# Performance work log

Hardware: AMD Instinct MI355X
Metric: run time of the kernel (lower is better)

Reference implementation:

```python
import jax, jax.numpy as jnp
import numpy as np

H, W = 6144, 6144
KH, KW = 3, 3


def setup_inputs() -> dict:
    key = jax.random.key(0)
    k1, k2, k3 = jax.random.split(key, 3)
    x = jax.random.normal(k1, (H, W), dtype=jnp.float32)
    kernel = jax.random.normal(k2, (KH, KW), dtype=jnp.float32)
    bias = jax.random.normal(k3, (1,), dtype=jnp.float32)
    return {"x": x, "kernel": kernel, "bias": bias}


def reference(x, kernel, bias):
    # Valid 2D cross-correlation (no kernel flip), identical math to the
    # per-pixel double loop: out[i,j] = sum(x[i:i+h, j:j+w] * kernel) + bias.
    lhs = x[None, None, :, :]            # [N=1, C=1, H, W]
    rhs = kernel[None, None, :, :]       # [O=1, I=1, h, w]
    out = jax.lax.conv_general_dilated(
        lhs, rhs,
        window_strides=(1, 1),
        padding="VALID",
        dimension_numbers=("NCHW", "OIHW", "NCHW"),
    )[0, 0]                              # [H-h+1, W-w+1]
    return out + bias[0]
```

## Files before the change

kernel.cpp:

```cpp
#include <hip/hip_runtime.h>


#define W_IN  6144
#define H_IN  6144
#define OW    6142
#define OH    6142
#define ROWS  4
#define NCOLT 1536

typedef float f32x2 __attribute__((ext_vector_type(2)));
typedef float f32x4 __attribute__((ext_vector_type(4)));

template <bool INTERIOR>
__device__ __forceinline__ void corr_body(const float* __restrict__ x,
                                          float* __restrict__ out,
                                          int c0, int r0,
                                          float k00, float k01, float k02,
                                          float k10, float k11, float k12,
                                          float k20, float k21, float k22,
                                          float bv)
{
    if (c0 + 4 <= OW) {
        float v[6][6];
#pragma unroll
        for (int r = 0; r < 6; ++r) {
            const int rr = r0 + r;
            if (INTERIOR || rr < H_IN) {
                const float* p = x + rr * W_IN + c0;
                const f32x4 a = *reinterpret_cast<const f32x4*>(p);
                const f32x2 c = *reinterpret_cast<const f32x2*>(p + 4);
                v[r][0] = a.x; v[r][1] = a.y; v[r][2] = a.z; v[r][3] = a.w;
                v[r][4] = c.x; v[r][5] = c.y;
            } else {
                v[r][0] = v[r][1] = v[r][2] = v[r][3] = v[r][4] = v[r][5] = 0.f;
            }
        }
#pragma unroll
        for (int m = 0; m < ROWS; ++m) {
            const int rr = r0 + m;
            if (INTERIOR || rr < OH) {
                float acc[4];
#pragma unroll
                for (int j = 0; j < 4; ++j) {
                    acc[j] = bv
                        + v[m + 0][j] * k00 + v[m + 0][j + 1] * k01 + v[m + 0][j + 2] * k02
                        + v[m + 1][j] * k10 + v[m + 1][j + 1] * k11 + v[m + 1][j + 2] * k12
                        + v[m + 2][j] * k20 + v[m + 2][j + 1] * k21 + v[m + 2][j + 2] * k22;
                }
                float* po = out + rr * OW + c0;
                f32x2 s0; s0.x = acc[0]; s0.y = acc[1];
                f32x2 s1; s1.x = acc[2]; s1.y = acc[3];
                __builtin_nontemporal_store(s0, reinterpret_cast<f32x2*>(po));
                __builtin_nontemporal_store(s1, reinterpret_cast<f32x2*>(po + 2));
            }
        }
    } else {
        float v[6][4];
#pragma unroll
        for (int r = 0; r < 6; ++r) {
            const int rr = r0 + r;
            if (INTERIOR || rr < H_IN) {
                const f32x4 a = *reinterpret_cast<const f32x4*>(x + rr * W_IN + c0);
                v[r][0] = a.x; v[r][1] = a.y; v[r][2] = a.z; v[r][3] = a.w;
            } else {
                v[r][0] = v[r][1] = v[r][2] = v[r][3] = 0.f;
            }
        }
#pragma unroll
        for (int m = 0; m < ROWS; ++m) {
            const int rr = r0 + m;
            if (INTERIOR || rr < OH) {
                float a0 = bv
                    + v[m + 0][0] * k00 + v[m + 0][1] * k01 + v[m + 0][2] * k02
                    + v[m + 1][0] * k10 + v[m + 1][1] * k11 + v[m + 1][2] * k12
                    + v[m + 2][0] * k20 + v[m + 2][1] * k21 + v[m + 2][2] * k22;
                float a1 = bv
                    + v[m + 0][1] * k00 + v[m + 0][2] * k01 + v[m + 0][3] * k02
                    + v[m + 1][1] * k10 + v[m + 1][2] * k11 + v[m + 1][3] * k12
                    + v[m + 2][1] * k20 + v[m + 2][2] * k21 + v[m + 2][3] * k22;
                f32x2 s0; s0.x = a0; s0.y = a1;
                __builtin_nontemporal_store(s0, reinterpret_cast<f32x2*>(out + rr * OW + c0));
            }
        }
    }
}

__global__ __launch_bounds__(256, 4)
void corr2d_kernel(const float* __restrict__ x,
                   const float* __restrict__ kk,
                   const float* __restrict__ bias,
                   float* __restrict__ out) {
    const int t  = blockIdx.x * 256 + threadIdx.x;
    const int c0 = t << 2;
    const int r0 = blockIdx.y * ROWS;

    const float k00 = kk[0], k01 = kk[1], k02 = kk[2];
    const float k10 = kk[3], k11 = kk[4], k12 = kk[5];
    const float k20 = kk[6], k21 = kk[7], k22 = kk[8];
    const float bv = bias[0];

    if (r0 + ROWS + 1 < H_IN) {
        corr_body<true>(x, out, c0, r0, k00, k01, k02, k10, k11, k12, k20, k21, k22, bv);
    } else {
        corr_body<false>(x, out, c0, r0, k00, k01, k02, k10, k11, k12, k20, k21, k22, bv);
    }
}

extern "C" void kernel_launch(void* const* d_in, const int* in_sizes, int n_in,
                              void* d_out, int out_size, void* d_ws, size_t ws_size,
                              hipStream_t stream) {
    const float* x    = (const float*)d_in[0];
    const float* k    = (const float*)d_in[1];
    const float* bias = (const float*)d_in[2];
    float* out        = (float*)d_out;

    dim3 block(256, 1, 1);
    dim3 grid(NCOLT / 256, (OH + ROWS - 1) / ROWS, 1);
    corr2d_kernel<<<grid, block, 0, stream>>>(x, k, bias, out);
}
```

Baseline: 60.55 us.

## Double rows per thread and remap workgroups per XCD for locality

Each thread now computes 8 output rows instead of 4, which cuts the halo re-read overhead from 6/4 to 10/8 input rows per output row. The grid is flattened to 1D and workgroup IDs are remapped so that consecutive workgroups dispatched to the same XCD cover adjacent row tiles, improving L2 sharing of halo rows. The occupancy hint in launch_bounds is dropped. Register use rises because each thread holds 10x6 input values.

```diff
diff --git a/kernel.cpp b/kernel.cpp
--- a/kernel.cpp
+++ b/kernel.cpp
@@ -5,14 +5,17 @@
 #define H_IN  6144
 #define OW    6142
 #define OH    6142
-#define ROWS  4
-#define NCOLT 1536
+#define ROWS  8
+#define GRID_X 6
+#define GRID_Y 768
+#define NWG   (GRID_X * GRID_Y)
+#define WG_PER_XCD (NWG / 8)
 
 typedef float f32x2 __attribute__((ext_vector_type(2)));
 typedef float f32x4 __attribute__((ext_vector_type(4)));
 
 template <bool INTERIOR>
-__device__ __forceinline__ void corr_body(const float* __restrict__ x,
+__device__ __forceinline__ void body_main(const float* __restrict__ x,
                                           float* __restrict__ out,
                                           int c0, int r0,
                                           float k00, float k01, float k02,
@@ -20,89 +23,110 @@
                                           float k20, float k21, float k22,
                                           float bv)
 {
-    if (c0 + 4 <= OW) {
-        float v[6][6];
+    float v[ROWS + 2][6];
 #pragma unroll
-        for (int r = 0; r < 6; ++r) {
-            const int rr = r0 + r;
-            if (INTERIOR || rr < H_IN) {
-                const float* p = x + rr * W_IN + c0;
-                const f32x4 a = *reinterpret_cast<const f32x4*>(p);
-                const f32x2 c = *reinterpret_cast<const f32x2*>(p + 4);
-                v[r][0] = a.x; v[r][1] = a.y; v[r][2] = a.z; v[r][3] = a.w;
-                v[r][4] = c.x; v[r][5] = c.y;
-            } else {
-                v[r][0] = v[r][1] = v[r][2] = v[r][3] = v[r][4] = v[r][5] = 0.f;
+    for (int r = 0; r < ROWS + 2; ++r) {
+        const int rr = r0 + r;
+        if (INTERIOR || rr < H_IN) {
+            const float* p = x + rr * W_IN + c0;
+            const f32x4 a = *reinterpret_cast<const f32x4*>(p);
+            const f32x2 c = *reinterpret_cast<const f32x2*>(p + 4);
+            v[r][0] = a.x; v[r][1] = a.y; v[r][2] = a.z; v[r][3] = a.w;
+            v[r][4] = c.x; v[r][5] = c.y;
+        } else {
+#pragma unroll
+            for (int j = 0; j < 6; ++j) v[r][j] = 0.f;
+        }
+    }
+
+#pragma unroll
+    for (int m = 0; m < ROWS; ++m) {
+        const int rr = r0 + m;
+        if (INTERIOR || rr < OH) {
+            float acc[4];
+#pragma unroll
+            for (int j = 0; j < 4; ++j) {
+                acc[j] = bv
+                    + v[m + 0][j] * k00 + v[m + 0][j + 1] * k01 + v[m + 0][j + 2] * k02
+                    + v[m + 1][j] * k10 + v[m + 1][j + 1] * k11 + v[m + 1][j + 2] * k12
+                    + v[m + 2][j] * k20 + v[m + 2][j + 1] * k21 + v[m + 2][j + 2] * k22;
             }
-        }
-#pragma unroll
-        for (int m = 0; m < ROWS; ++m) {
-            const int rr = r0 + m;
-            if (INTERIOR || rr < OH) {
-                float acc[4];
-#pragma unroll
-                for (int j = 0; j < 4; ++j) {
-                    acc[j] = bv
-                        + v[m + 0][j] * k00 + v[m + 0][j + 1] * k01 + v[m + 0][j + 2] * k02
-                        + v[m + 1][j] * k10 + v[m + 1][j + 1] * k11 + v[m + 1][j + 2] * k12
-                        + v[m + 2][j] * k20 + v[m + 2][j + 1] * k21 + v[m + 2][j + 2] * k22;
-                }
-                float* po = out + rr * OW + c0;
-                f32x2 s0; s0.x = acc[0]; s0.y = acc[1];
-                f32x2 s1; s1.x = acc[2]; s1.y = acc[3];
-                __builtin_nontemporal_store(s0, reinterpret_cast<f32x2*>(po));
-                __builtin_nontemporal_store(s1, reinterpret_cast<f32x2*>(po + 2));
-            }
-        }
-    } else {
-        float v[6][4];
-#pragma unroll
-        for (int r = 0; r < 6; ++r) {
-            const int rr = r0 + r;
-            if (INTERIOR || rr < H_IN) {
-                const f32x4 a = *reinterpret_cast<const f32x4*>(x + rr * W_IN + c0);
-                v[r][0] = a.x; v[r][1] = a.y; v[r][2] = a.z; v[r][3] = a.w;
-            } else {
-                v[r][0] = v[r][1] = v[r][2] = v[r][3] = 0.f;
-            }
-        }
-#pragma unroll
-        for (int m = 0; m < ROWS; ++m) {
-            const int rr = r0 + m;
-            if (INTERIOR || rr < OH) {
-                float a0 = bv
-                    + v[m + 0][0] * k00 + v[m + 0][1] * k01 + v[m + 0][2] * k02
-                    + v[m + 1][0] * k10 + v[m + 1][1] * k11 + v[m + 1][2] * k12
-                    + v[m + 2][0] * k20 + v[m + 2][1] * k21 + v[m + 2][2] * k22;
-                float a1 = bv
-                    + v[m + 0][1] * k00 + v[m + 0][2] * k01 + v[m + 0][3] * k02
-                    + v[m + 1][1] * k10 + v[m + 1][2] * k11 + v[m + 1][3] * k12
-                    + v[m + 2][1] * k20 + v[m + 2][2] * k21 + v[m + 2][3] * k22;
-                f32x2 s0; s0.x = a0; s0.y = a1;
-                __builtin_nontemporal_store(s0, reinterpret_cast<f32x2*>(out + rr * OW + c0));
-            }
+            float* po = out + rr * OW + c0;
+            f32x2 s0; s0.x = acc[0]; s0.y = acc[1];
+            f32x2 s1; s1.x = acc[2]; s1.y = acc[3];
+            __builtin_nontemporal_store(s0, reinterpret_cast<f32x2*>(po));
+            __builtin_nontemporal_store(s1, reinterpret_cast<f32x2*>(po + 2));
         }
     }
 }
 
-__global__ __launch_bounds__(256, 4)
+template <bool INTERIOR>
+__device__ __forceinline__ void body_tail(const float* __restrict__ x,
+                                          float* __restrict__ out,
+                                          int c0, int r0,
+                                          float k00, float k01, float k02,
+                                          float k10, float k11, float k12,
+                                          float k20, float k21, float k22,
+                                          float bv)
+{
+    float v[ROWS + 2][4];
+#pragma unroll
+    for (int r = 0; r < ROWS + 2; ++r) {
+        const int rr = r0 + r;
+        if (INTERIOR || rr < H_IN) {
+            const f32x4 a = *reinterpret_cast<const f32x4*>(x + rr * W_IN + c0);
+            v[r][0] = a.x; v[r][1] = a.y; v[r][2] = a.z; v[r][3] = a.w;
+        } else {
+#pragma unroll
+            for (int j = 0; j < 4; ++j) v[r][j] = 0.f;
+        }
+    }
+
+#pragma unroll
+    for (int m = 0; m < ROWS; ++m) {
+        const int rr = r0 + m;
+        if (INTERIOR || rr < OH) {
+            float a0 = bv
+                + v[m + 0][0] * k00 + v[m + 0][1] * k01 + v[m + 0][2] * k02
+                + v[m + 1][0] * k10 + v[m + 1][1] * k11 + v[m + 1][2] * k12
+                + v[m + 2][0] * k20 + v[m + 2][1] * k21 + v[m + 2][2] * k22;
+            float a1 = bv
+                + v[m + 0][1] * k00 + v[m + 0][2] * k01 + v[m + 0][3] * k02
+                + v[m + 1][1] * k10 + v[m + 1][2] * k11 + v[m + 1][3] * k12
+                + v[m + 2][1] * k20 + v[m + 2][2] * k21 + v[m + 2][3] * k22;
+            f32x2 s0; s0.x = a0; s0.y = a1;
+            __builtin_nontemporal_store(s0, reinterpret_cast<f32x2*>(out + rr * OW + c0));
+        }
+    }
+}
+
+__global__ __launch_bounds__(256)
 void corr2d_kernel(const float* __restrict__ x,
                    const float* __restrict__ kk,
                    const float* __restrict__ bias,
                    float* __restrict__ out) {
-    const int t  = blockIdx.x * 256 + threadIdx.x;
+    const int id = blockIdx.x;
+    const int wg = (id & 7) * WG_PER_XCD + (id >> 3);
+    const int bx = wg / GRID_Y;
+    const int by = wg - bx * GRID_Y;
+
+    const int t  = bx * 256 + (int)threadIdx.x;
     const int c0 = t << 2;
-    const int r0 = blockIdx.y * ROWS;
+    const int r0 = by * ROWS;
 
     const float k00 = kk[0], k01 = kk[1], k02 = kk[2];
     const float k10 = kk[3], k11 = kk[4], k12 = kk[5];
     const float k20 = kk[6], k21 = kk[7], k22 = kk[8];
     const float bv = bias[0];
 
-    if (r0 + ROWS + 1 < H_IN) {
-        corr_body<true>(x, out, c0, r0, k00, k01, k02, k10, k11, k12, k20, k21, k22, bv);
+    const bool interior = (r0 + ROWS + 1) < H_IN;
+
+    if (c0 + 4 <= OW) {
+        if (interior) body_main<true >(x, out, c0, r0, k00, k01, k02, k10, k11, k12, k20, k21, k22, bv);
+        else          body_main<false>(x, out, c0, r0, k00, k01, k02, k10, k11, k12, k20, k21, k22, bv);
     } else {
-        corr_body<false>(x, out, c0, r0, k00, k01, k02, k10, k11, k12, k20, k21, k22, bv);
+        if (interior) body_tail<true >(x, out, c0, r0, k00, k01, k02, k10, k11, k12, k20, k21, k22, bv);
+        else          body_tail<false>(x, out, c0, r0, k00, k01, k02, k10, k11, k12, k20, k21, k22, bv);
     }
 }
 
@@ -115,6 +139,6 @@
     float* out        = (float*)d_out;
 
     dim3 block(256, 1, 1);
-    dim3 grid(NCOLT / 256, (OH + ROWS - 1) / ROWS, 1);
+    dim3 grid(NWG, 1, 1);
     corr2d_kernel<<<grid, block, 0, stream>>>(x, k, bias, out);
 }
```

Result: faster. 51.12 us, median of 2 (-15.6%).
